# Performance work log

Measured on AMD Instinct MI355X. Metric: run time of the kernel, lower is better.

Reference implementation:

```python
import jax, jax.numpy as jnp
import numpy as np

B, S, HID = 2, 2048, 2048
NH, NKV, HD = 16, 4, 128
ROT = 64            # head_dim * partial_rotary_factor
WINDOW = 512        # sliding_window_size
ROPE_BASE = 10000.0


def setup_inputs() -> dict:
    key = jax.random.key(0)
    ks = jax.random.split(key, 5)
    scale = 0.02
    return {
        "hidden_states": jax.random.normal(ks[0], (B, S, HID), jnp.float32),
        "Wq": jax.random.normal(ks[1], (NH * HD, HID), jnp.float32) * scale,
        "Wk": jax.random.normal(ks[2], (NKV * HD, HID), jnp.float32) * scale,
        "Wv": jax.random.normal(ks[3], (NKV * HD, HID), jnp.float32) * scale,
        "Wo": jax.random.normal(ks[4], (HID, NH * HD), jnp.float32) * scale,
    }


def _rope_cos_sin(seq_len, dtype):
    inv_freq = 1.0 / (ROPE_BASE ** (jnp.arange(0, ROT, 2, dtype=jnp.float32) / ROT))
    t = jnp.arange(seq_len, dtype=jnp.float32)
    freqs = t[:, None] * inv_freq[None, :]          # [S, ROT/2]
    emb = jnp.concatenate([freqs, freqs], axis=-1)   # [S, ROT]
    return jnp.cos(emb).astype(dtype), jnp.sin(emb).astype(dtype)


def _rotate_half(x):
    x1, x2 = x[..., : x.shape[-1] // 2], x[..., x.shape[-1] // 2:]
    return jnp.concatenate([-x2, x1], axis=-1)


def reference(hidden_states, Wq, Wk, Wv, Wo):
    b, s, _ = hidden_states.shape
    n_rep = NH // NKV

    q = (hidden_states @ Wq.T).reshape(b, s, NH, HD).transpose(0, 2, 1, 3)    # [B,NH,S,HD]
    k = (hidden_states @ Wk.T).reshape(b, s, NKV, HD).transpose(0, 2, 1, 3)   # [B,NKV,S,HD]
    v = (hidden_states @ Wv.T).reshape(b, s, NKV, HD).transpose(0, 2, 1, 3)

    # partial rotary embedding on the first ROT dims
    cos, sin = _rope_cos_sin(s, q.dtype)   # [S, ROT]
    cos = cos[None, None]                  # broadcast over batch, heads
    sin = sin[None, None]
    q_rot, q_pass = q[..., :ROT], q[..., ROT:]
    k_rot, k_pass = k[..., :ROT], k[..., ROT:]
    q_rot = q_rot * cos + _rotate_half(q_rot) * sin
    k_rot = k_rot * cos + _rotate_half(k_rot) * sin
    q = jnp.concatenate([q_rot, q_pass], axis=-1)
    k = jnp.concatenate([k_rot, k_pass], axis=-1)

    # GQA: repeat kv heads
    k = jnp.repeat(k, n_rep, axis=1)   # [B,NH,S,HD]
    v = jnp.repeat(v, n_rep, axis=1)

    scores = jnp.einsum("bhqd,bhkd->bhqk", q, k) / jnp.sqrt(jnp.asarray(HD, q.dtype))

    # sliding-window causal mask: allow j in [i-WINDOW+1, i]
    i = jnp.arange(s)[:, None]
    j = jnp.arange(s)[None, :]
    allowed = (j <= i) & (j > i - WINDOW)
    scores = jnp.where(allowed[None, None], scores, -jnp.inf)

    attn = jax.nn.softmax(scores.astype(jnp.float32), axis=-1).astype(q.dtype)
    out = jnp.einsum("bhqk,bhkd->bhqd", attn, v)          # [B,NH,S,HD]
    out = out.transpose(0, 2, 1, 3).reshape(b, s, NH * HD)
    return out @ Wo.T
```

## Files before the change

kernel.cpp:

```cpp
#include <hip/hip_runtime.h>
#include <cstdint>
#include <cstddef>

typedef __bf16 bf16;
typedef __attribute__((ext_vector_type(8))) __bf16 bf16x8;
typedef __attribute__((ext_vector_type(4))) __bf16 bf16x4;
typedef __attribute__((ext_vector_type(4))) float f32x4;
typedef __attribute__((ext_vector_type(4))) short s16x4;

#define S_LEN   2048
#define WIN     512
#define NH_Q    16
#define NH_KV   4
#define HD_     128
#define NTOK    4096

#if defined(__has_builtin)
#if __has_builtin(__builtin_amdgcn_mfma_f32_16x16x16bf16_1k)
#define HAVE_MFMA16 1
#endif
#endif
#ifndef HAVE_MFMA16
#define HAVE_MFMA16 0
#endif

#define WAIT_VM4   0x0F74
#define WAIT_VM3   0x0F73
#define WAIT_VM2   0x0F72
#define WAIT_VM0   0x0F70
#define CFENCE() __asm__ __volatile__("" ::: "memory")

__device__ __forceinline__ void async_copy16(const void* g, void* l) {
  __builtin_amdgcn_global_load_lds(
      (const __attribute__((address_space(1))) void*)g,
      (__attribute__((address_space(3))) void*)l, 16, 0, 0);
}

__global__ __launch_bounds__(256)
void cvt_all(const float* __restrict__ hs, const float* __restrict__ wq,
             const float* __restrict__ wk, const float* __restrict__ wv,
             const float* __restrict__ wo, bf16* __restrict__ hsb,
             bf16* __restrict__ wqb, bf16* __restrict__ wkb,
             bf16* __restrict__ wvb, bf16* __restrict__ wob) {
  long i = ((long)blockIdx.x * 256 + threadIdx.x) * 4;
  const float* in;
  bf16* out;
  if (i < 8388608)       { in = hs + i;            out = hsb + i; }
  else if (i < 12582912) { in = wq + (i - 8388608); out = wqb + (i - 8388608); }
  else if (i < 13631488) { in = wk + (i - 12582912); out = wkb + (i - 12582912); }
  else if (i < 14680064) { in = wv + (i - 13631488); out = wvb + (i - 13631488); }
  else                   { in = wo + (i - 14680064); out = wob + (i - 14680064); }
  float4 v = *(const float4*)in;
  bf16x4 t = {(bf16)v.x, (bf16)v.y, (bf16)v.z, (bf16)v.w};
  *(bf16x4*)out = t;
}

__global__ __launch_bounds__(512, 2)
void gemm_out8(const bf16* __restrict__ A, const bf16* __restrict__ W,
               float* __restrict__ C) {
  __shared__ __align__(16) char smem[98304];
  const int tid  = threadIdx.x;
  const int wave = tid >> 6, lane = tid & 63;
  const int quad = lane >> 4, l16 = lane & 15;
  const int wm = wave >> 1, wn = wave & 1;

  const int flat = blockIdx.y * 16 + blockIdx.x;
  const int swz  = (flat & 7) * 32 + (flat >> 3);
  const int m0 = (swz >> 4) * 256;
  const int n0 = (swz & 15) * 128;

  const int rdb = (l16 * 64 + quad * 16) ^ ((l16 & 8) << 2);
  const int srow = lane >> 2;
  const int scol = ((lane & 3) * 8) ^ ((lane >> 5) << 4);

  const bf16* aptr[2][2];
  int adst[2][2];
#pragma unroll
  for (int mh = 0; mh < 2; ++mh)
#pragma unroll
    for (int j = 0; j < 2; ++j) {
      const int rb = (wave >> 1) * 4 + mh * 2 + j;
      aptr[mh][j] = A + (size_t)(m0 + rb * 16 + srow) * 2048 + scol
                    + (wave & 1) * 32;
      adst[mh][j] = (rb * 2 + (wave & 1)) << 10;
    }
  const bf16* bptr[2];
  int bdst[2];
#pragma unroll
  for (int nh = 0; nh < 2; ++nh) {
    const int cb = (wave >> 2) * 4 + nh * 2 + ((wave >> 1) & 1);
    bptr[nh] = W + (size_t)(n0 + cb * 16 + srow) * 2048 + scol
               + (wave & 1) * 32;
    bdst[nh] = (cb * 2 + (wave & 1)) << 10;
  }

#define STAGE_A(mh, tt) do { char* _b = smem + ((tt) & 1) * 32768;      \
    async_copy16(aptr[mh][0] + (tt) * 64, _b + adst[mh][0]);            \
    async_copy16(aptr[mh][1] + (tt) * 64, _b + adst[mh][1]); } while (0)
#define STAGE_B(nh, tt) do { char* _b = smem + 65536 + ((tt) & 1) * 16384; \
    async_copy16(bptr[nh] + (tt) * 64, _b + bdst[nh]); } while (0)

  f32x4 acc[4][4];
#pragma unroll
  for (int i = 0; i < 4; ++i)
#pragma unroll
    for (int j = 0; j < 4; ++j) acc[i][j] = (f32x4){0.f, 0.f, 0.f, 0.f};

  bf16x8 afr[2][2];
  bf16x8 bfr[2][2][2];

  auto read_a = [&](const char* Ab, int mh) __attribute__((always_inline)) {
#pragma unroll
    for (int mt2 = 0; mt2 < 2; ++mt2)
#pragma unroll
      for (int ks = 0; ks < 2; ++ks)
        afr[mt2][ks] = *(const bf16x8*)(
            Ab + (((wm * 4 + mh * 2 + mt2) * 2 + ks) << 10) + rdb);
  };
  auto read_b = [&](const char* Bb, int nh) __attribute__((always_inline)) {
#pragma unroll
    for (int nt2 = 0; nt2 < 2; ++nt2)
#pragma unroll
      for (int ks = 0; ks < 2; ++ks)
        bfr[nh][nt2][ks] = *(const bf16x8*)(
            Bb + (((wn * 4 + nh * 2 + nt2) * 2 + ks) << 10) + rdb);
  };
  auto do_mfma = [&](int mh, int nh) __attribute__((always_inline)) {
    __builtin_amdgcn_s_setprio(1);
#pragma unroll
    for (int mt2 = 0; mt2 < 2; ++mt2)
#pragma unroll
      for (int nt2 = 0; nt2 < 2; ++nt2)
#pragma unroll
        for (int ks = 0; ks < 2; ++ks)
          acc[mh * 2 + mt2][nh * 2 + nt2] = __builtin_amdgcn_mfma_f32_16x16x32_bf16(
              afr[mt2][ks], bfr[nh][nt2][ks], acc[mh * 2 + mt2][nh * 2 + nt2],
              0, 0, 0);
    __builtin_amdgcn_s_setprio(0);
  };

  STAGE_A(0, 0); STAGE_B(0, 0); STAGE_B(1, 0); STAGE_A(1, 0);
  CFENCE();

  for (int t = 0; t < 31; ++t) {
    const char* Ab = smem + (t & 1) * 32768;
    const char* Bb = smem + 65536 + (t & 1) * 16384;
    const int nx = t + 1;
    __builtin_amdgcn_s_waitcnt(WAIT_VM3); CFENCE();
    __builtin_amdgcn_s_barrier(); CFENCE();
    read_a(Ab, 0); read_b(Bb, 0);
    STAGE_A(0, nx); CFENCE();
    do_mfma(0, 0);
    __builtin_amdgcn_s_waitcnt(WAIT_VM4); CFENCE();
    __builtin_amdgcn_s_barrier(); CFENCE();
    read_b(Bb, 1);
    STAGE_B(0, nx); CFENCE();
    do_mfma(0, 1);
    __builtin_amdgcn_s_waitcnt(WAIT_VM3); CFENCE();
    __builtin_amdgcn_s_barrier(); CFENCE();
    read_a(Ab, 1);
    STAGE_B(1, nx); CFENCE();
    do_mfma(1, 0);
    __builtin_amdgcn_s_barrier(); CFENCE();
    STAGE_A(1, nx); CFENCE();
    do_mfma(1, 1);
  }
  {
    const char* Ab = smem + 32768;
    const char* Bb = smem + 65536 + 16384;
    __builtin_amdgcn_s_waitcnt(WAIT_VM3); CFENCE();
    __builtin_amdgcn_s_barrier(); CFENCE();
    read_a(Ab, 0); read_b(Bb, 0);
    do_mfma(0, 0);
    __builtin_amdgcn_s_waitcnt(WAIT_VM2); CFENCE();
    __builtin_amdgcn_s_barrier(); CFENCE();
    read_b(Bb, 1);
    do_mfma(0, 1);
    __builtin_amdgcn_s_waitcnt(WAIT_VM0); CFENCE();
    __builtin_amdgcn_s_barrier(); CFENCE();
    read_a(Ab, 1);
    do_mfma(1, 0);
    do_mfma(1, 1);
  }
#undef STAGE_A
#undef STAGE_B

#pragma unroll
  for (int mt = 0; mt < 4; ++mt)
#pragma unroll
    for (int nt = 0; nt < 4; ++nt)
#pragma unroll
      for (int r = 0; r < 4; ++r) {
        const int row = m0 + wm * 64 + mt * 16 + quad * 4 + r;
        const int col = n0 + wn * 64 + nt * 16 + l16;
        C[(size_t)row * 2048 + col] = acc[mt][nt][r];
      }
}

__global__ __launch_bounds__(512, 2)
void gemm_qkv9(const bf16* __restrict__ A, const bf16* __restrict__ Wq,
               const bf16* __restrict__ Wk, const bf16* __restrict__ Wv,
               bf16* __restrict__ Qo, bf16* __restrict__ Ko,
               bf16* __restrict__ Vt) {
  __shared__ __align__(16) char smem[114688];
  const int tid  = threadIdx.x;
  const int wave = tid >> 6, lane = tid & 63;
  const int quad = lane >> 4, l16 = lane & 15;
  const int wm = wave >> 1, wn = wave & 1;

  const int flat = blockIdx.y * 16 + blockIdx.x;
  const int swz  = (flat & 7) * 32 + (flat >> 3);
  const int m0 = (swz >> 4) * 256;
  const int n0 = (swz & 15) * 192;

  const int rdb = (l16 * 64 + quad * 16) ^ ((l16 & 8) << 2);

  const int srow = lane >> 2;
  const int scol = ((lane & 3) * 8) ^ ((lane >> 5) << 4);

  const int rbA0 = (wave >> 1) * 4 + (wave & 1);
  const int rbA1 = rbA0 + 2;
  const bf16* a0p = A + (size_t)(m0 + rbA0 * 16 + srow) * 2048 + scol;
  const bf16* a1p = A + (size_t)(m0 + rbA1 * 16 + srow) * 2048 + scol;
  const int da0 = (rbA0 * 2) << 10;
  const int da1 = (rbA1 * 2) << 10;

  const int rbB0 = wave >> 1, khB0 = wave & 1;
  const int rbB1 = 4 + wave;
  const int nrow0 = n0 + rbB0 * 16 + srow;
  const int nrow1 = n0 + rbB1 * 16 + srow;
  const bf16* b0p = (nrow0 < 2048 ? Wq + (size_t)nrow0 * 2048
                   : nrow0 < 2560 ? Wk + (size_t)(nrow0 - 2048) * 2048
                                  : Wv + (size_t)(nrow0 - 2560) * 2048)
                    + scol + khB0 * 32;
  const bf16* b1p = (nrow1 < 2048 ? Wq + (size_t)nrow1 * 2048
                   : nrow1 < 2560 ? Wk + (size_t)(nrow1 - 2048) * 2048
                                  : Wv + (size_t)(nrow1 - 2560) * 2048)
                    + scol;
  const int db0 = (rbB0 * 2 + khB0) << 10;
  const int db1 = (rbB1 * 2) << 10;

#define STAGE_A0(tt) do { char* _b = smem + ((tt) & 1) * 32768;        \
    async_copy16(a0p + (tt) * 64,      _b + da0);                      \
    async_copy16(a0p + (tt) * 64 + 32, _b + da0 + 1024); } while (0)
#define STAGE_A1(tt) do { char* _b = smem + ((tt) & 1) * 32768;        \
    async_copy16(a1p + (tt) * 64,      _b + da1);                      \
    async_copy16(a1p + (tt) * 64 + 32, _b + da1 + 1024); } while (0)
#define STAGE_B0(tt) do { char* _b = smem + 65536 + ((tt) & 1) * 24576; \
    async_copy16(b0p + (tt) * 64,      _b + db0); } while (0)
#define STAGE_B12(tt) do { char* _b = smem + 65536 + ((tt) & 1) * 24576; \
    async_copy16(b1p + (tt) * 64,      _b + db1);                      \
    async_copy16(b1p + (tt) * 64 + 32, _b + db1 + 1024); } while (0)

  f32x4 acc[4][6];
#pragma unroll
  for (int i = 0; i < 4; ++i)
#pragma unroll
    for (int j = 0; j < 6; ++j) acc[i][j] = (f32x4){0.f, 0.f, 0.f, 0.f};

  bf16x8 afr[2][2];
  bf16x8 bfr[6][2];

  auto read_a = [&](const char* Ab, int mh) __attribute__((always_inline)) {
#pragma unroll
    for (int mt2 = 0; mt2 < 2; ++mt2)
#pragma unroll
      for (int ks = 0; ks < 2; ++ks)
        afr[mt2][ks] = *(const bf16x8*)(
            Ab + (((wm * 4 + mh * 2 + mt2) * 2 + ks) << 10) + rdb);
  };
  auto read_b = [&](const char* Bb, int jlo, int jhi) __attribute__((always_inline)) {
#pragma unroll
    for (int j = 0; j < 6; ++j) {
      if (j < jlo || j > jhi) continue;
      const int cc = (j >> 1) * 4 + (j & 1) * 2 + wn;
#pragma unroll
      for (int ks = 0; ks < 2; ++ks)
        bfr[j][ks] = *(const bf16x8*)(Bb + ((cc * 2 + ks) << 10) + rdb);
    }
  };
  auto do_mfma = [&](int mh, int jlo, int jhi) __attribute__((always_inline)) {
    __builtin_amdgcn_s_setprio(1);
#pragma unroll
    for (int mt2 = 0; mt2 < 2; ++mt2)
#pragma unroll
      for (int j = 0; j < 6; ++j) {
        if (j < jlo || j > jhi) continue;
#pragma unroll
        for (int ks = 0; ks < 2; ++ks)
          acc[mh * 2 + mt2][j] = __builtin_amdgcn_mfma_f32_16x16x32_bf16(
              afr[mt2][ks], bfr[j][ks], acc[mh * 2 + mt2][j], 0, 0, 0);
      }
    __builtin_amdgcn_s_setprio(0);
  };

  STAGE_A0(0); STAGE_B0(0); STAGE_B12(0); STAGE_A1(0);
  CFENCE();

  for (int t = 0; t < 31; ++t) {
    const char* Ab = smem + (t & 1) * 32768;
    const char* Bb = smem + 65536 + (t & 1) * 24576;
    const int nx = t + 1;
    __builtin_amdgcn_s_waitcnt(WAIT_VM4); CFENCE();
    __builtin_amdgcn_s_barrier(); CFENCE();
    read_a(Ab, 0); read_b(Bb, 0, 1);
    STAGE_A0(nx); CFENCE();
    do_mfma(0, 0, 1);
    __builtin_amdgcn_s_waitcnt(WAIT_VM4); CFENCE();
    __builtin_amdgcn_s_barrier(); CFENCE();
    read_b(Bb, 2, 5);
    STAGE_B0(nx); CFENCE();
    do_mfma(0, 2, 5);
    __builtin_amdgcn_s_waitcnt(WAIT_VM3); CFENCE();
    __builtin_amdgcn_s_barrier(); CFENCE();
    read_a(Ab, 1);
    STAGE_B12(nx); CFENCE();
    do_mfma(1, 0, 1);
    __builtin_amdgcn_s_barrier(); CFENCE();
    STAGE_A1(nx); CFENCE();
    do_mfma(1, 2, 5);
  }
  {
    const char* Ab = smem + 32768;
    const char* Bb = smem + 65536 + 24576;
    __builtin_amdgcn_s_waitcnt(WAIT_VM4); CFENCE();
    __builtin_amdgcn_s_barrier(); CFENCE();
    read_a(Ab, 0); read_b(Bb, 0, 1);
    do_mfma(0, 0, 1);
    __builtin_amdgcn_s_waitcnt(WAIT_VM2); CFENCE();
    __builtin_amdgcn_s_barrier(); CFENCE();
    read_b(Bb, 2, 5);
    do_mfma(0, 2, 5);
    __builtin_amdgcn_s_waitcnt(WAIT_VM0); CFENCE();
    __builtin_amdgcn_s_barrier(); CFENCE();
    read_a(Ab, 1);
    do_mfma(1, 0, 1);
    do_mfma(1, 2, 5);
  }
#undef STAGE_A0
#undef STAGE_A1
#undef STAGE_B0
#undef STAGE_B12

  {
    const float d = (float)(wn * 16 + l16);
    const float invf = exp2f(-d * 0.41524101186091903f);
#pragma unroll
    for (int b = 0; b < 3; ++b) {
      const int cb = n0 + b * 64;
      if (cb < 2560 && (cb & 127) == 0) {
#pragma unroll
        for (int mt = 0; mt < 4; ++mt)
#pragma unroll
          for (int r = 0; r < 4; ++r) {
            const int pos = (m0 + wm * 64 + mt * 16 + quad * 4 + r) & (S_LEN - 1);
            float s, c;
            __sincosf((float)pos * invf, &s, &c);
            const float x1 = acc[mt][2 * b][r], x2 = acc[mt][2 * b + 1][r];
            acc[mt][2 * b][r]     = x1 * c - x2 * s;
            acc[mt][2 * b + 1][r] = x2 * c + x1 * s;
          }
      }
    }
  }
#pragma unroll
  for (int mt = 0; mt < 4; ++mt) {
    const int row0 = m0 + wm * 64 + mt * 16 + quad * 4;
#pragma unroll
    for (int j = 0; j < 6; ++j) {
      const int col16 = n0 + (j >> 1) * 64 + ((j & 1) * 2 + wn) * 16;
      if (col16 < 2048) {
#pragma unroll
        for (int r = 0; r < 4; ++r)
          Qo[(size_t)(row0 + r) * 2048 + col16 + l16] = (bf16)acc[mt][j][r];
      } else if (col16 < 2560) {
#pragma unroll
        for (int r = 0; r < 4; ++r)
          Ko[(size_t)(row0 + r) * 512 + col16 - 2048 + l16] = (bf16)acc[mt][j][r];
      } else {
        const int colv = col16 + l16 - 2560;
        const int bb = row0 >> 11, s0 = row0 & (S_LEN - 1);
        bf16x4 tq = {(bf16)acc[mt][j][0], (bf16)acc[mt][j][1],
                     (bf16)acc[mt][j][2], (bf16)acc[mt][j][3]};
        *(bf16x4*)(Vt + ((size_t)(bb * NH_KV + (colv >> 7)) * HD_ + (colv & 127))
                        * S_LEN + s0) = tq;
      }
    }
  }
}

#define KS_STRIDE 136
#define VT_STRIDE 72

__global__ __launch_bounds__(256)
void attn_kernel(const bf16* __restrict__ Qg, const bf16* __restrict__ Kg,
                 const bf16* __restrict__ Vtg, bf16* __restrict__ Og) {
  __shared__ __align__(16) bf16 Ks[64 * KS_STRIDE];
  __shared__ __align__(16) bf16 Vt[128 * VT_STRIDE];
#if !HAVE_MFMA16
  __shared__ __align__(16) bf16 Pb[4][16 * 72];
#endif
  const int tid  = threadIdx.x;
  const int wave = tid >> 6, lane = tid & 63;
  const int quad = lane >> 4, l16 = lane & 15;
  const int qt = blockIdx.x, h = blockIdx.y, b = blockIdx.z;
  const int kv = h >> 2;
  const int q0 = qt * 64;
  const int tok0 = b * S_LEN;
  const float scale = 0.08838834764831845f;
  const int q = q0 + wave * 16 + l16;

  bf16x8 qf[4];
  {
    const bf16* qp = Qg + (size_t)(tok0 + q) * (NH_Q * HD_) + h * HD_ + quad * 8;
#pragma unroll
    for (int kb = 0; kb < 4; ++kb) qf[kb] = *(const bf16x8*)(qp + kb * 32);
  }

  f32x4 o[8];
#pragma unroll
  for (int dt = 0; dt < 8; ++dt) o[dt] = (f32x4){0.f, 0.f, 0.f, 0.f};
  float m_run = -__builtin_inff(), l_run = 0.f;

  int kt_begin = q0 - WIN;
  if (kt_begin < 0) kt_begin = 0;
  const int kt_end = q0 + 64;
  const bf16* vt_base = Vtg + (size_t)(b * NH_KV + kv) * HD_ * S_LEN;

  for (int kt = kt_begin; kt < kt_end; kt += 64) {
    __syncthreads();
#pragma unroll
    for (int it = 0; it < 4; ++it) {
      int vid = tid + it * 256;
      int key = vid >> 4, dblk = vid & 15;
      bf16x8 v = *(const bf16x8*)(Kg + (size_t)(tok0 + kt + key) * (NH_KV * HD_)
                                  + kv * HD_ + dblk * 8);
      *(bf16x8*)&Ks[key * KS_STRIDE + dblk * 8] = v;
    }
#pragma unroll
    for (int it = 0; it < 4; ++it) {
      int vid = tid + it * 256;
      int d = vid >> 3, kblk = vid & 7;
      bf16x8 v = *(const bf16x8*)(vt_base + (size_t)d * S_LEN + kt + kblk * 8);
      *(bf16x8*)&Vt[d * VT_STRIDE + kblk * 8] = v;
    }
    __syncthreads();

    f32x4 st[4];
#pragma unroll
    for (int nt = 0; nt < 4; ++nt) {
      f32x4 acc = (f32x4){0.f, 0.f, 0.f, 0.f};
#pragma unroll
      for (int kb = 0; kb < 4; ++kb) {
        bf16x8 kf = *(const bf16x8*)&Ks[(nt * 16 + l16) * KS_STRIDE + kb * 32 + quad * 8];
        acc = __builtin_amdgcn_mfma_f32_16x16x32_bf16(kf, qf[kb], acc, 0, 0, 0);
      }
      st[nt] = acc;
    }
#pragma unroll
    for (int nt = 0; nt < 4; ++nt)
#pragma unroll
      for (int r = 0; r < 4; ++r) {
        int key = kt + nt * 16 + quad * 4 + r;
        bool ok = (key <= q) && (key > q - WIN);
        st[nt][r] = ok ? st[nt][r] * scale : -__builtin_inff();
      }
    float mx = -__builtin_inff();
#pragma unroll
    for (int nt = 0; nt < 4; ++nt)
#pragma unroll
      for (int r = 0; r < 4; ++r) mx = fmaxf(mx, st[nt][r]);
    mx = fmaxf(mx, __shfl_xor(mx, 16, 64));
    mx = fmaxf(mx, __shfl_xor(mx, 32, 64));
    float mnew = fmaxf(m_run, mx);
    float msub = (mnew == -__builtin_inff()) ? 0.f : mnew;
    float alpha = __expf(m_run - msub);
    m_run = mnew;
    float p[4][4], psum = 0.f;
#pragma unroll
    for (int nt = 0; nt < 4; ++nt)
#pragma unroll
      for (int r = 0; r < 4; ++r) {
        p[nt][r] = __expf(st[nt][r] - msub);
        psum += p[nt][r];
      }
    psum += __shfl_xor(psum, 16, 64);
    psum += __shfl_xor(psum, 32, 64);
    l_run = l_run * alpha + psum;
#pragma unroll
    for (int dt = 0; dt < 8; ++dt) o[dt] *= alpha;

#if HAVE_MFMA16
    s16x4 pb[4];
#pragma unroll
    for (int nt = 0; nt < 4; ++nt)
#pragma unroll
      for (int r = 0; r < 4; ++r) {
        union { __bf16 h; short s; } u;
        u.h = (bf16)p[nt][r];
        pb[nt][r] = u.s;
      }
#pragma unroll
    for (int dt = 0; dt < 8; ++dt)
#pragma unroll
      for (int nt = 0; nt < 4; ++nt) {
        s16x4 vf = *(const s16x4*)&Vt[(dt * 16 + l16) * VT_STRIDE + nt * 16 + quad * 4];
        o[dt] = __builtin_amdgcn_mfma_f32_16x16x16bf16_1k(vf, pb[nt], o[dt], 0, 0, 0);
      }
#else
#pragma unroll
    for (int nt = 0; nt < 4; ++nt) {
      bf16x4 t;
#pragma unroll
      for (int r = 0; r < 4; ++r) t[r] = (bf16)p[nt][r];
      *(bf16x4*)&Pb[wave][l16 * 72 + nt * 16 + quad * 4] = t;
    }
    __syncthreads();
    bf16x8 pf[2];
    pf[0] = *(const bf16x8*)&Pb[wave][l16 * 72 + quad * 8];
    pf[1] = *(const bf16x8*)&Pb[wave][l16 * 72 + 32 + quad * 8];
#pragma unroll
    for (int dt = 0; dt < 8; ++dt)
#pragma unroll
      for (int kb = 0; kb < 2; ++kb) {
        bf16x8 vf = *(const bf16x8*)&Vt[(dt * 16 + l16) * VT_STRIDE + kb * 32 + quad * 8];
        o[dt] = __builtin_amdgcn_mfma_f32_16x16x32_bf16(vf, pf[kb], o[dt], 0, 0, 0);
      }
#endif
  }

  float inv = 1.f / l_run;
  __syncthreads();
#pragma unroll
  for (int dt = 0; dt < 8; ++dt) {
    bf16x4 t;
#pragma unroll
    for (int r = 0; r < 4; ++r) t[r] = (bf16)(o[dt][r] * inv);
    *(bf16x4*)&Ks[(wave * 16 + l16) * KS_STRIDE + dt * 16 + quad * 4] = t;
  }
  __syncthreads();
#pragma unroll
  for (int it = 0; it < 4; ++it) {
    int idx = tid + it * 256;
    int row = idx >> 4, chunk = idx & 15;
    bf16x8 v = *(const bf16x8*)&Ks[row * KS_STRIDE + chunk * 8];
    *(bf16x8*)(Og + (size_t)(tok0 + q0 + row) * (NH_Q * HD_) + h * HD_ + chunk * 8) = v;
  }
}

extern "C" void kernel_launch(void* const* d_in, const int* in_sizes, int n_in,
                              void* d_out, int out_size, void* d_ws, size_t ws_size,
                              hipStream_t stream) {
  const float* hs = (const float*)d_in[0];
  const float* Wq = (const float*)d_in[1];
  const float* Wk = (const float*)d_in[2];
  const float* Wv = (const float*)d_in[3];
  const float* Wo = (const float*)d_in[4];
  float* out = (float*)d_out;

  char* w = (char*)d_ws;
  bf16* hsb = (bf16*)w; w += (size_t)NTOK * 2048 * 2;
  bf16* wqb = (bf16*)w; w += (size_t)2048 * 2048 * 2;
  bf16* wkb = (bf16*)w; w += (size_t)512 * 2048 * 2;
  bf16* wvb = (bf16*)w; w += (size_t)512 * 2048 * 2;
  bf16* wob = (bf16*)w; w += (size_t)2048 * 2048 * 2;
  bf16* qb  = (bf16*)w; w += (size_t)NTOK * 2048 * 2;
  bf16* kb  = (bf16*)w; w += (size_t)NTOK * 512 * 2;
  bf16* vtb = (bf16*)w; w += (size_t)NTOK * 512 * 2;
  bf16* ab  = hsb;

  cvt_all<<<18874368 / 1024, 256, 0, stream>>>(hs, Wq, Wk, Wv, Wo,
                                               hsb, wqb, wkb, wvb, wob);

  gemm_qkv9<<<dim3(16, 16), 512, 0, stream>>>(hsb, wqb, wkb, wvb,
                                              qb, kb, vtb);

  attn_kernel<<<dim3(S_LEN / 64, NH_Q, 2), 256, 0, stream>>>(qb, kb, vtb, ab);

  gemm_out8<<<dim3(16, 16), 512, 0, stream>>>(ab, wob, out);
}
```

Measured before the change: 244.2 us.

## Restructure attention: 128-query blocks, register prefetch, exp2 with folded scale, lazy rescale

The attention kernel now uses 512-thread blocks covering 128 queries, so each K/V tile loaded into shared memory serves twice as many queries. The next K/V tile is prefetched into registers while the current one is computed, and blocks are swizzled across the grid. The softmax scale times log2(e) is folded into Q in the QKV GEMM epilogue so exp2 can be used directly. Waves skip tiles outside their window, apply masks only on edge tiles, and rescale the accumulators only when the running max grows by more than 8. The cost is more registers per thread, extra wave priority hints, and a small bf16 precision shift from pre-scaling Q.

```diff
diff --git a/kernel.cpp b/kernel.cpp
--- a/kernel.cpp
+++ b/kernel.cpp
@@ -14,6 +14,8 @@
 #define NH_KV   4
 #define HD_     128
 #define NTOK    4096
+
+#define QSCALE_LOG2E 0.12751744561823337f
 
 #if defined(__has_builtin)
 #if __has_builtin(__builtin_amdgcn_mfma_f32_16x16x16bf16_1k)
@@ -214,7 +216,6 @@
   const int n0 = (swz & 15) * 192;
 
   const int rdb = (l16 * 64 + quad * 16) ^ ((l16 & 8) << 2);
-
   const int srow = lane >> 2;
   const int scol = ((lane & 3) * 8) ^ ((lane >> 5) << 4);
 
@@ -372,7 +373,8 @@
       if (col16 < 2048) {
 #pragma unroll
         for (int r = 0; r < 4; ++r)
-          Qo[(size_t)(row0 + r) * 2048 + col16 + l16] = (bf16)acc[mt][j][r];
+          Qo[(size_t)(row0 + r) * 2048 + col16 + l16] =
+              (bf16)(acc[mt][j][r] * QSCALE_LOG2E);
       } else if (col16 < 2560) {
 #pragma unroll
         for (int r = 0; r < 4; ++r)
@@ -392,23 +394,27 @@
 #define KS_STRIDE 136
 #define VT_STRIDE 72
 
-__global__ __launch_bounds__(256)
+__global__ __launch_bounds__(512, 4)
 void attn_kernel(const bf16* __restrict__ Qg, const bf16* __restrict__ Kg,
                  const bf16* __restrict__ Vtg, bf16* __restrict__ Og) {
-  __shared__ __align__(16) bf16 Ks[64 * KS_STRIDE];
-  __shared__ __align__(16) bf16 Vt[128 * VT_STRIDE];
-#if !HAVE_MFMA16
-  __shared__ __align__(16) bf16 Pb[4][16 * 72];
-#endif
+  __shared__ __align__(16) char smem_raw[35840];
+  bf16* const Ks = (bf16*)smem_raw;
+  bf16* const Vt = (bf16*)(smem_raw + 17408);
+  bf16* const Os = (bf16*)smem_raw;
+
   const int tid  = threadIdx.x;
   const int wave = tid >> 6, lane = tid & 63;
   const int quad = lane >> 4, l16 = lane & 15;
-  const int qt = blockIdx.x, h = blockIdx.y, b = blockIdx.z;
+
+  const int flat = blockIdx.x + 16 * blockIdx.y + 256 * blockIdx.z;
+  const int swz  = (flat & 7) * 64 + (flat >> 3);
+  const int qt = swz & 15, h = (swz >> 4) & 15, b = swz >> 8;
+
   const int kv = h >> 2;
-  const int q0 = qt * 64;
+  const int q0 = qt * 128;
   const int tok0 = b * S_LEN;
-  const float scale = 0.08838834764831845f;
-  const int q = q0 + wave * 16 + l16;
+  const int qw = q0 + wave * 16;
+  const int q  = qw + l16;
 
   bf16x8 qf[4];
   {
@@ -424,29 +430,41 @@
 
   int kt_begin = q0 - WIN;
   if (kt_begin < 0) kt_begin = 0;
-  const int kt_end = q0 + 64;
+  const int kt_end = q0 + 128;
+  const bf16* kg_base = Kg + (size_t)tok0 * (NH_KV * HD_) + kv * HD_;
   const bf16* vt_base = Vtg + (size_t)(b * NH_KV + kv) * HD_ * S_LEN;
 
+  const int skey = tid >> 4, sdbl = tid & 15;
+  const int svd  = tid >> 3, skb  = tid & 7;
+
+  bf16x8 pk0, pk1, pv0, pv1;
+  auto PF = [&](int kt) __attribute__((always_inline)) {
+    pk0 = *(const bf16x8*)(kg_base + (size_t)(kt + skey) * (NH_KV * HD_) + sdbl * 8);
+    pk1 = *(const bf16x8*)(kg_base + (size_t)(kt + skey + 32) * (NH_KV * HD_) + sdbl * 8);
+    pv0 = *(const bf16x8*)(vt_base + (size_t)svd * S_LEN + kt + skb * 8);
+    pv1 = *(const bf16x8*)(vt_base + (size_t)(svd + 64) * S_LEN + kt + skb * 8);
+  };
+  auto WR = [&]() __attribute__((always_inline)) {
+    *(bf16x8*)&Ks[skey * KS_STRIDE + sdbl * 8] = pk0;
+    *(bf16x8*)&Ks[(skey + 32) * KS_STRIDE + sdbl * 8] = pk1;
+    *(bf16x8*)&Vt[svd * VT_STRIDE + skb * 8] = pv0;
+    *(bf16x8*)&Vt[(svd + 64) * VT_STRIDE + skb * 8] = pv1;
+  };
+
+  PF(kt_begin);
   for (int kt = kt_begin; kt < kt_end; kt += 64) {
     __syncthreads();
-#pragma unroll
-    for (int it = 0; it < 4; ++it) {
-      int vid = tid + it * 256;
-      int key = vid >> 4, dblk = vid & 15;
-      bf16x8 v = *(const bf16x8*)(Kg + (size_t)(tok0 + kt + key) * (NH_KV * HD_)
-                                  + kv * HD_ + dblk * 8);
-      *(bf16x8*)&Ks[key * KS_STRIDE + dblk * 8] = v;
-    }
-#pragma unroll
-    for (int it = 0; it < 4; ++it) {
-      int vid = tid + it * 256;
-      int d = vid >> 3, kblk = vid & 7;
-      bf16x8 v = *(const bf16x8*)(vt_base + (size_t)d * S_LEN + kt + kblk * 8);
-      *(bf16x8*)&Vt[d * VT_STRIDE + kblk * 8] = v;
-    }
+    WR();
     __syncthreads();
-
-    f32x4 st[4];
+    if (kt + 64 < kt_end) PF(kt + 64);
+
+    const bool active = (kt <= qw + 15) && (kt + 63 > qw - WIN);
+    if (!active) continue;
+    const bool need_c = (kt + 63 > qw);
+    const bool need_l = (kt + WIN <= qw + 15);
+
+    f32x4 st4[4];
+    __builtin_amdgcn_s_setprio(1);
 #pragma unroll
     for (int nt = 0; nt < 4; ++nt) {
       f32x4 acc = (f32x4){0.f, 0.f, 0.f, 0.f};
@@ -455,51 +473,59 @@
         bf16x8 kf = *(const bf16x8*)&Ks[(nt * 16 + l16) * KS_STRIDE + kb * 32 + quad * 8];
         acc = __builtin_amdgcn_mfma_f32_16x16x32_bf16(kf, qf[kb], acc, 0, 0, 0);
       }
-      st[nt] = acc;
-    }
+      st4[nt] = acc;
+    }
+    __builtin_amdgcn_s_setprio(0);
+
+    if (need_c || need_l) {
+#pragma unroll
+      for (int nt = 0; nt < 4; ++nt)
+#pragma unroll
+        for (int r = 0; r < 4; ++r) {
+          const int key = kt + nt * 16 + quad * 4 + r;
+          const bool ok = (!need_c || key <= q) && (!need_l || key > q - WIN);
+          st4[nt][r] = ok ? st4[nt][r] : -__builtin_inff();
+        }
+    }
+
+    float mx = -__builtin_inff();
 #pragma unroll
     for (int nt = 0; nt < 4; ++nt)
 #pragma unroll
-      for (int r = 0; r < 4; ++r) {
-        int key = kt + nt * 16 + quad * 4 + r;
-        bool ok = (key <= q) && (key > q - WIN);
-        st[nt][r] = ok ? st[nt][r] * scale : -__builtin_inff();
-      }
-    float mx = -__builtin_inff();
-#pragma unroll
-    for (int nt = 0; nt < 4; ++nt)
-#pragma unroll
-      for (int r = 0; r < 4; ++r) mx = fmaxf(mx, st[nt][r]);
+      for (int r = 0; r < 4; ++r) mx = fmaxf(mx, st4[nt][r]);
     mx = fmaxf(mx, __shfl_xor(mx, 16, 64));
     mx = fmaxf(mx, __shfl_xor(mx, 32, 64));
-    float mnew = fmaxf(m_run, mx);
-    float msub = (mnew == -__builtin_inff()) ? 0.f : mnew;
-    float alpha = __expf(m_run - msub);
-    m_run = mnew;
-    float p[4][4], psum = 0.f;
+
+    float msub;
+    if (!__all(mx - m_run <= 8.f)) {
+      const float mnew = fmaxf(m_run, mx);
+      msub = (mnew == -__builtin_inff()) ? 0.f : mnew;
+      const float alpha = __builtin_amdgcn_exp2f(m_run - msub);
+      l_run *= alpha;
+#pragma unroll
+      for (int dt = 0; dt < 8; ++dt) o[dt] *= alpha;
+      m_run = mnew;
+    } else {
+      msub = m_run;
+    }
+
+    float psum = 0.f;
+    s16x4 pb[4];
 #pragma unroll
     for (int nt = 0; nt < 4; ++nt)
 #pragma unroll
       for (int r = 0; r < 4; ++r) {
-        p[nt][r] = __expf(st[nt][r] - msub);
-        psum += p[nt][r];
+        const float pv = __builtin_amdgcn_exp2f(st4[nt][r] - msub);
+        psum += pv;
+        union { __bf16 hh; short ss; } u;
+        u.hh = (bf16)pv;
+        pb[nt][r] = u.ss;
       }
     psum += __shfl_xor(psum, 16, 64);
     psum += __shfl_xor(psum, 32, 64);
-    l_run = l_run * alpha + psum;
-#pragma unroll
-    for (int dt = 0; dt < 8; ++dt) o[dt] *= alpha;
-
-#if HAVE_MFMA16
-    s16x4 pb[4];
-#pragma unroll
-    for (int nt = 0; nt < 4; ++nt)
-#pragma unroll
-      for (int r = 0; r < 4; ++r) {
-        union { __bf16 h; short s; } u;
-        u.h = (bf16)p[nt][r];
-        pb[nt][r] = u.s;
-      }
+    l_run += psum;
+
+    __builtin_amdgcn_s_setprio(1);
 #pragma unroll
     for (int dt = 0; dt < 8; ++dt)
 #pragma unroll
@@ -507,43 +533,24 @@
         s16x4 vf = *(const s16x4*)&Vt[(dt * 16 + l16) * VT_STRIDE + nt * 16 + quad * 4];
         o[dt] = __builtin_amdgcn_mfma_f32_16x16x16bf16_1k(vf, pb[nt], o[dt], 0, 0, 0);
       }
-#else
-#pragma unroll
-    for (int nt = 0; nt < 4; ++nt) {
-      bf16x4 t;
-#pragma unroll
-      for (int r = 0; r < 4; ++r) t[r] = (bf16)p[nt][r];
-      *(bf16x4*)&Pb[wave][l16 * 72 + nt * 16 + quad * 4] = t;
-    }
-    __syncthreads();
-    bf16x8 pf[2];
-    pf[0] = *(const bf16x8*)&Pb[wave][l16 * 72 + quad * 8];
-    pf[1] = *(const bf16x8*)&Pb[wave][l16 * 72 + 32 + quad * 8];
-#pragma unroll
-    for (int dt = 0; dt < 8; ++dt)
-#pragma unroll
-      for (int kb = 0; kb < 2; ++kb) {
-        bf16x8 vf = *(const bf16x8*)&Vt[(dt * 16 + l16) * VT_STRIDE + kb * 32 + quad * 8];
-        o[dt] = __builtin_amdgcn_mfma_f32_16x16x32_bf16(vf, pf[kb], o[dt], 0, 0, 0);
-      }
-#endif
-  }
-
-  float inv = 1.f / l_run;
+    __builtin_amdgcn_s_setprio(0);
+  }
+
+  const float inv = 1.f / l_run;
   __syncthreads();
 #pragma unroll
   for (int dt = 0; dt < 8; ++dt) {
     bf16x4 t;
 #pragma unroll
     for (int r = 0; r < 4; ++r) t[r] = (bf16)(o[dt][r] * inv);
-    *(bf16x4*)&Ks[(wave * 16 + l16) * KS_STRIDE + dt * 16 + quad * 4] = t;
+    *(bf16x4*)&Os[(wave * 16 + l16) * KS_STRIDE + dt * 16 + quad * 4] = t;
   }
   __syncthreads();
 #pragma unroll
   for (int it = 0; it < 4; ++it) {
-    int idx = tid + it * 256;
-    int row = idx >> 4, chunk = idx & 15;
-    bf16x8 v = *(const bf16x8*)&Ks[row * KS_STRIDE + chunk * 8];
+    const int idx = tid + it * 512;
+    const int row = idx >> 4, chunk = idx & 15;
+    bf16x8 v = *(const bf16x8*)&Os[row * KS_STRIDE + chunk * 8];
     *(bf16x8*)(Og + (size_t)(tok0 + q0 + row) * (NH_Q * HD_) + h * HD_ + chunk * 8) = v;
   }
 }
@@ -575,7 +582,7 @@
   gemm_qkv9<<<dim3(16, 16), 512, 0, stream>>>(hsb, wqb, wkb, wvb,
                                               qb, kb, vtb);
 
-  attn_kernel<<<dim3(S_LEN / 64, NH_Q, 2), 256, 0, stream>>>(qb, kb, vtb, ab);
+  attn_kernel<<<dim3(S_LEN / 128, NH_Q, 2), 512, 0, stream>>>(qb, kb, vtb, ab);
 
   gemm_out8<<<dim3(16, 16), 512, 0, stream>>>(ab, wob, out);
 }
```

After: 233.7 us. 4.3% less time.
